# Kernel tuning notes

Hardware: AMD Instinct MI355X
Metric: run time of the kernel (lower is better)

Reference implementation:

```python
import jax, jax.numpy as jnp
import numpy as np

B = 8192       # number of windows (batch*windows_per_image)
N = 49         # tokens per 7x7 window
C = 128        # channels
H = 4          # heads
HD = C // H    # head dim = 32
WIN = (7, 7)


def _relative_position_index(win):
    wh, ww = win
    coords = np.stack(np.meshgrid(np.arange(wh), np.arange(ww), indexing='ij'))
    cf = coords.reshape(2, -1)                       # (2, N)
    rel = (cf[:, :, None] - cf[:, None, :]).transpose(1, 2, 0)  # (N, N, 2)
    rel[:, :, 0] += wh - 1
    rel[:, :, 1] += ww - 1
    rel[:, :, 0] *= 2 * ww - 1
    return jnp.array(rel.sum(-1).reshape(-1), dtype=jnp.int32)  # (N*N,)


def setup_inputs() -> dict:
    key = jax.random.key(0)
    ks = jax.random.split(key, 7)
    x = jax.random.normal(ks[0], (B, N, C), dtype=jnp.float32)
    mask = jax.random.normal(ks[1], (B, 1, N, N), dtype=jnp.float32)
    qkv_w = jax.random.normal(ks[2], (C, 3 * C), dtype=jnp.float32) * (C ** -0.5)
    qkv_b = jnp.zeros((3 * C,), dtype=jnp.float32)
    rel_bias_table = jax.random.normal(ks[3], ((2 * WIN[0] - 1) * (2 * WIN[1] - 1), H), dtype=jnp.float32)
    proj_w = jax.random.normal(ks[4], (C, C), dtype=jnp.float32) * (C ** -0.5)
    proj_b = jnp.zeros((C,), dtype=jnp.float32)
    rel_index = _relative_position_index(WIN)
    return {"x": x, "mask": mask, "qkv_w": qkv_w, "qkv_b": qkv_b,
            "rel_bias_table": rel_bias_table, "proj_w": proj_w,
            "proj_b": proj_b, "rel_index": rel_index}


def reference(x, mask, qkv_w, qkv_b, rel_bias_table, proj_w, proj_b, rel_index):
    b, n, c = x.shape
    scale = HD ** -0.5
    qkv = (x @ qkv_w + qkv_b).reshape(b, n, 3, H, HD).transpose(2, 0, 3, 1, 4)
    q, k, v = qkv[0] * scale, qkv[1], qkv[2]          # (b, H, n, HD)
    attn = jnp.einsum('bhqd,bhkd->bhqk', q, k)        # (b, H, n, n)
    # gathered relative position bias: (n*n, H) -> (1, H, n, n)
    bias = rel_bias_table[rel_index].reshape(n, n, H).transpose(2, 0, 1)[None]
    attn = jax.nn.softmax(attn + bias + mask, axis=-1)
    out = jnp.einsum('bhqk,bhkd->bhqd', attn, v)       # (b, H, n, HD)
    out = out.transpose(0, 2, 1, 3).reshape(b, n, c)
    return out @ proj_w + proj_b
```

## Files before the change

### kernel.cpp

```cpp
#include <hip/hip_runtime.h>
#include <hip/hip_bf16.h>

using f32x4 = __attribute__((ext_vector_type(4))) float;
using bf16x8 = __attribute__((ext_vector_type(8))) short;

#define DEVI __device__ __forceinline__

DEVI short f2bf(float f) { __hip_bfloat16 h = __float2bfloat16(f); return *reinterpret_cast<short*>(&h); }
DEVI unsigned int pk2(float a, float b) {
    float2 t; t.x = a; t.y = b;
    __hip_bfloat162 h = __float22bfloat162_rn(t);
    return *reinterpret_cast<unsigned int*>(&h);
}
DEVI float bf2f(unsigned short s) { unsigned int u = ((unsigned int)s) << 16; return __uint_as_float(u); }

DEVI void pl32swap(unsigned& a, unsigned& b) { asm("v_permlane32_swap_b32 %0, %1" : "+v"(a), "+v"(b)); }
DEVI void pl16swap(unsigned& a, unsigned& b) { asm("v_permlane16_swap_b32 %0, %1" : "+v"(a), "+v"(b)); }

#define GLOAD_LDS16(gp, lp) \
    __builtin_amdgcn_global_load_lds((const __attribute__((address_space(1))) void*)(gp), \
                                     (__attribute__((address_space(3))) void*)(lp), 16, 0, 0)

constexpr int NB = 8192;
constexpr int NT = 49;
constexpr int CD = 128;
constexpr float SCALE = 0.17677669529663687f;
constexpr float LOG2E = 1.4426950408889634f;

constexpr size_t WS_QKVWS  = 0;
constexpr size_t WS_PROJWT = 98304;
constexpr size_t WS_BIAS   = 131072;

DEVI void div49(unsigned grow, unsigned& bI, unsigned& tI) {
    bI = (unsigned)(((unsigned long long)grow * 2804876602ull) >> 37);
    tI = grow - bI * 49u;
}

DEVI int swz128(int row, int col) { return row * 128 + (col ^ ((row & 7) << 3)); }

__global__ __launch_bounds__(256) void prep_kernel(
    const float* __restrict__ qkv_w, const float* __restrict__ proj_w,
    const float* __restrict__ rbt, const int* __restrict__ rel_index,
    short* __restrict__ qkvwS, short* __restrict__ projwT, unsigned short* __restrict__ biasBf)
{
    int i = blockIdx.x * 256 + threadIdx.x;
    if (i < 384 * 128) {
        int n = i >> 7, j = i & 127;
        int c = n >> 7, r = n & 127;
        qkvwS[c * 16384 + r * 128 + (j ^ ((r & 7) << 3))] = f2bf(qkv_w[j * 384 + n]);
    }
    if (i < 128 * 128) {
        int n = i >> 7, j = i & 127;
        projwT[n * 128 + j] = f2bf(proj_w[j * 128 + n]);
    }
    if (i < 4 * NT * NT) {
        int h = i / (NT * NT); int t = i % (NT * NT);
        int k = t / NT, q = t - k * NT;
        biasBf[i] = (unsigned short)f2bf(rbt[rel_index[q * NT + k] * 4 + h] * LOG2E);
    }
}

__global__ __launch_bounds__(512, 4) void fused_kernel(
    const float* __restrict__ x, const float* __restrict__ mask,
    const float* __restrict__ qkv_b, const short* __restrict__ qkvwS,
    const unsigned short* __restrict__ biasT, const short* __restrict__ projwT,
    const float* __restrict__ proj_b, float* __restrict__ out)
{
    __shared__ __attribute__((aligned(16))) short pool[40960];
    char*  Wcb = (char*)pool;
    char*  qkb = (char*)pool + 32768;
    char*  vSb = (char*)pool + 65536;
    float* mT  = (float*)pool;
    short* oS  = (short*)((char*)pool + 49152);

    const int b = blockIdx.x;
    const int tid = threadIdx.x;
    const int w = tid >> 6, lane = tid & 63, lr = lane & 15, lg = lane >> 4;
    const int h = w >> 1, half = w & 1;
    const int wpair = w >> 1;
    const int tsel = w & 1;

    const float* mb_ = mask + (size_t)b * (NT * NT);
    float mreg[5];
#pragma unroll
    for (int ii = 0; ii < 5; ++ii) {
        int i = tid + ii * 512;
        mreg[ii] = (i < NT * NT) ? mb_[i] * LOG2E : 0.f;
    }

    bf16x8 af[2][4];
#pragma unroll
    for (int mf = 0; mf < 2; ++mf) {
        const int row = 32 * tsel + 16 * mf + lr;
        const bool valid = row < NT;
        const float* xrow = x + ((size_t)b * NT + (valid ? row : 0)) * CD;
#pragma unroll
        for (int kt = 0; kt < 4; ++kt) {
            float4 v0 = {0.f,0.f,0.f,0.f}, v1 = {0.f,0.f,0.f,0.f};
            if (valid) {
                const float4* p = reinterpret_cast<const float4*>(xrow + kt * 32 + lg * 8);
                v0 = p[0]; v1 = p[1];
            }
            union { unsigned int u[4]; bf16x8 v; } cv;
            cv.u[0] = pk2(v0.x, v0.y); cv.u[1] = pk2(v0.z, v0.w);
            cv.u[2] = pk2(v1.x, v1.y); cv.u[3] = pk2(v1.z, v1.w);
            af[mf][kt] = cv.v;
        }
    }

    const char* srcW = (const char*)qkvwS;
#pragma unroll
    for (int c = 0; c < 3; ++c) {
#pragma unroll
        for (int i = 0; i < 4; ++i)
            GLOAD_LDS16(srcW + c * 32768 + w * 4096 + i * 1024 + lane * 16,
                        Wcb + w * 4096 + i * 1024);
        __syncthreads();

        if (c < 2) {
#pragma unroll
            for (int nn = 0; nn < 2; ++nn) {
                const int ntl = wpair + 4 * nn;
                const int nt = c * 8 + ntl;
                const int hh = (ntl >> 1) & 3;
                const int dtile = ntl & 1;
                const float4 b4 = *reinterpret_cast<const float4*>(qkv_b + nt * 16 + 4 * lg);
                const float scl = (c == 0) ? SCALE * LOG2E : 1.0f;
                const char* wbase = Wcb + (ntl * 16 + lr) * 256;
                const int wsw = (lr & 7) << 4;
#pragma unroll
                for (int tf = 0; tf < 2; ++tf) {
                    f32x4 acc = {0.f, 0.f, 0.f, 0.f};
#pragma unroll
                    for (int kt = 0; kt < 4; ++kt) {
                        bf16x8 wf = *reinterpret_cast<const bf16x8*>(wbase + ((kt * 64 + lg * 16) ^ wsw));
                        acc = __builtin_amdgcn_mfma_f32_16x16x32_bf16(wf, af[tf][kt], acc, 0, 0, 0);
                    }
                    const int t = 16 * (2 * tsel + tf) + lr;
                    const int gp = (dtile * 4 + lg) ^ (t & 6);
                    uint2 s;
                    s.x = pk2((acc[0] + b4.x) * scl, (acc[1] + b4.y) * scl);
                    s.y = pk2((acc[2] + b4.z) * scl, (acc[3] + b4.w) * scl);
                    *reinterpret_cast<uint2*>(qkb + c * 16384 + hh * 4096 + t * 64 + gp * 8) = s;
                }
            }
        } else {
#pragma unroll
            for (int nn = 0; nn < 2; ++nn) {
                const int ntl = wpair + 4 * nn;
                const int nt = 16 + ntl;
                const int hh = (ntl >> 1) & 3;
                const int d0 = (ntl & 1) * 16;
                const float bv = qkv_b[nt * 16 + lr];
                const int d = d0 + lr;
                const char* wbase = Wcb + (ntl * 16 + lr) * 256;
                const int wsw = (lr & 7) << 4;
#pragma unroll
                for (int tf = 0; tf < 2; ++tf) {
                    f32x4 acc = {0.f, 0.f, 0.f, 0.f};
#pragma unroll
                    for (int kt = 0; kt < 4; ++kt) {
                        bf16x8 wf = *reinterpret_cast<const bf16x8*>(wbase + ((kt * 64 + lg * 16) ^ wsw));
                        acc = __builtin_amdgcn_mfma_f32_16x16x32_bf16(af[tf][kt], wf, acc, 0, 0, 0);
                    }
                    const int tt = 2 * tsel + tf;
                    const int slotq = (lg < 2) ? (tt * 8 + 4 * lg) : (24 + tt * 8 + 4 * lg);
                    const int gp = (slotq >> 2) ^ ((d & 7) << 1);
                    uint2 s;
                    s.x = pk2(acc[0] + bv, acc[1] + bv);
                    s.y = pk2(acc[2] + bv, acc[3] + bv);
                    *reinterpret_cast<uint2*>(vSb + hh * 4096 + d * 128 + gp * 8) = s;
                }
            }
        }
        __syncthreads();
    }

    const int mt0 = 2 * half;
    bf16x8 qa[2], kb[4];
#pragma unroll
    for (int i = 0; i < 2; ++i) {
        const int t = 16 * (mt0 + i) + lr;
        qa[i] = *reinterpret_cast<const bf16x8*>(qkb + h * 4096 + t * 64 + ((16 * lg) ^ ((t & 6) << 3)));
    }
#pragma unroll
    for (int t4 = 0; t4 < 4; ++t4) {
        const int t = 16 * t4 + lr;
        kb[t4] = *reinterpret_cast<const bf16x8*>(qkb + 16384 + h * 4096 + t * 64 + ((16 * lg) ^ ((t & 6) << 3)));
    }
#pragma unroll
    for (int ii = 0; ii < 5; ++ii) {
        int i = tid + ii * 512;
        if (i < NT * NT) {
            unsigned q_, k_;
            div49((unsigned)i, q_, k_);
            mT[k_ * 65 + q_] = mreg[ii];
        }
    }
    __syncthreads();

    const unsigned short* biasTh = biasT + h * (NT * NT);
    const short* vSs = (short*)vSb + h * 2048;
    const int sw8 = (lr & 7) << 3;

    f32x4 oacc[2][2];
#pragma unroll
    for (int mt2 = 0; mt2 < 2; ++mt2) { oacc[mt2][0] = f32x4{0,0,0,0}; oacc[mt2][1] = f32x4{0,0,0,0}; }

#pragma unroll
    for (int mt2 = 0; mt2 < 2; ++mt2) {
        const int qcol = 16 * (mt0 + mt2) + lr;

        float mbb[4][4];
#pragma unroll
        for (int ct = 0; ct < 4; ++ct)
#pragma unroll
            for (int r = 0; r < 4; ++r) {
                int k = 16 * ct + 4 * lg + r;
                int kc = min(k, 49);
                mbb[ct][r] = mT[kc * 65 + qcol] + bf2f(biasTh[kc * NT + qcol]);
            }

        f32x4 sacc[4];
#pragma unroll
        for (int ct = 0; ct < 4; ++ct) {
            f32x4 z = {0.f, 0.f, 0.f, 0.f};
            sacc[ct] = __builtin_amdgcn_mfma_f32_16x16x32_bf16(kb[ct], qa[mt2], z, 0, 0, 0);
        }

        float e[4][4];
        float psum = 0.f;
#pragma unroll
        for (int ct = 0; ct < 4; ++ct)
#pragma unroll
            for (int r = 0; r < 4; ++r) {
                float ee = exp2f(sacc[ct][r] + mbb[ct][r]);
                if (ct == 3) ee = (r == 0 && lg == 0) ? ee : 0.f;
                e[ct][r] = ee;
                psum += ee;
            }
        psum += __shfl_xor(psum, 16);
        psum += __shfl_xor(psum, 32);
        const float inv = 1.0f / psum;

        unsigned A0 = pk2(e[0][0] * inv, e[0][1] * inv);
        unsigned A1 = pk2(e[1][0] * inv, e[1][1] * inv);
        unsigned A2 = pk2(e[2][0] * inv, e[2][1] * inv);
        unsigned A3 = pk2(e[3][0] * inv, e[3][1] * inv);
        unsigned B0 = pk2(e[0][2] * inv, e[0][3] * inv);
        unsigned B1 = pk2(e[1][2] * inv, e[1][3] * inv);
        unsigned B2 = pk2(e[2][2] * inv, e[2][3] * inv);
        unsigned B3 = pk2(e[3][2] * inv, e[3][3] * inv);
        pl32swap(A0, A2); pl32swap(A1, A3);
        pl16swap(A0, A1); pl16swap(A2, A3);
        pl32swap(B0, B2); pl32swap(B1, B3);
        pl16swap(B0, B1); pl16swap(B2, B3);
        union { unsigned u[4]; bf16x8 v; } p0, p1;
        p0.u[0] = A0; p0.u[1] = B0; p0.u[2] = A1; p0.u[3] = B1;
        p1.u[0] = A2; p1.u[1] = B2; p1.u[2] = A3; p1.u[3] = B3;

#pragma unroll
        for (int nt = 0; nt < 2; ++nt) {
            bf16x8 vb0 = *reinterpret_cast<const bf16x8*>(&vSs[(16 * nt + lr) * 64 + ((8 * lg) ^ sw8)]);
            bf16x8 vb1 = *reinterpret_cast<const bf16x8*>(&vSs[(16 * nt + lr) * 64 + ((32 + 8 * lg) ^ sw8)]);
            oacc[mt2][nt] = __builtin_amdgcn_mfma_f32_16x16x32_bf16(p0.v, vb0, oacc[mt2][nt], 0, 0, 0);
            oacc[mt2][nt] = __builtin_amdgcn_mfma_f32_16x16x32_bf16(p1.v, vb1, oacc[mt2][nt], 0, 0, 0);
        }
    }

#pragma unroll
    for (int mt2 = 0; mt2 < 2; ++mt2)
#pragma unroll
        for (int nt = 0; nt < 2; ++nt)
#pragma unroll
            for (int r = 0; r < 4; ++r) {
                int row = 16 * (mt0 + mt2) + 4 * lg + r;
                int col = 32 * h + 16 * nt + lr;
                oS[swz128(row, col)] = f2bf(oacc[mt2][nt][r]);
            }
    __syncthreads();

    {
        bf16x8 bbf[4];
        const short* brow = projwT + (w * 16 + lr) * 128 + lg * 8;
#pragma unroll
        for (int kt = 0; kt < 4; ++kt)
            bbf[kt] = *reinterpret_cast<const bf16x8*>(brow + kt * 32);

        f32x4 acc[4];
#pragma unroll
        for (int mf = 0; mf < 4; ++mf) acc[mf] = f32x4{0.f, 0.f, 0.f, 0.f};

#pragma unroll
        for (int mf = 0; mf < 4; ++mf)
#pragma unroll
            for (int kt = 0; kt < 4; ++kt) {
                bf16x8 a2 = *reinterpret_cast<const bf16x8*>(&oS[swz128(16 * mf + lr, kt * 32 + lg * 8)]);
                acc[mf] = __builtin_amdgcn_mfma_f32_16x16x32_bf16(a2, bbf[kt], acc[mf], 0, 0, 0);
            }

        const int col = w * 16 + lr;
        const float pb = proj_b[col];
#pragma unroll
        for (int mf = 0; mf < 4; ++mf)
#pragma unroll
            for (int r = 0; r < 4; ++r) {
                int row = 16 * mf + 4 * lg + r;
                if (row < NT)
                    out[((size_t)b * NT + row) * CD + col] = acc[mf][r] + pb;
            }
    }
}

extern "C" void kernel_launch(void* const* d_in, const int* in_sizes, int n_in,
                              void* d_out, int out_size, void* d_ws, size_t ws_size,
                              hipStream_t stream) {
    const float* x      = (const float*)d_in[0];
    const float* mask   = (const float*)d_in[1];
    const float* qkv_w  = (const float*)d_in[2];
    const float* qkv_b  = (const float*)d_in[3];
    const float* rbt    = (const float*)d_in[4];
    const float* proj_w = (const float*)d_in[5];
    const float* proj_b = (const float*)d_in[6];
    const int*   ridx   = (const int*)d_in[7];
    float* out = (float*)d_out;

    char* ws = (char*)d_ws;
    short* qkvwS  = (short*)(ws + WS_QKVWS);
    short* projwT = (short*)(ws + WS_PROJWT);
    unsigned short* biasBf = (unsigned short*)(ws + WS_BIAS);

    prep_kernel<<<192, 256, 0, stream>>>(qkv_w, proj_w, rbt, ridx, qkvwS, projwT, biasBf);
    fused_kernel<<<NB, 512, 0, stream>>>(x, mask, qkv_b, qkvwS, biasBf, projwT, proj_b, out);
}
```

Baseline: 292.6 us.

## Load mask and bias directly into registers, drop LDS mask transpose

```diff
diff --git a/kernel.cpp b/kernel.cpp
--- a/kernel.cpp
+++ b/kernel.cpp
@@ -30,11 +30,6 @@
 constexpr size_t WS_QKVWS  = 0;
 constexpr size_t WS_PROJWT = 98304;
 constexpr size_t WS_BIAS   = 131072;
-
-DEVI void div49(unsigned grow, unsigned& bI, unsigned& tI) {
-    bI = (unsigned)(((unsigned long long)grow * 2804876602ull) >> 37);
-    tI = grow - bI * 49u;
-}
 
 DEVI int swz128(int row, int col) { return row * 128 + (col ^ ((row & 7) << 3)); }
 
@@ -70,7 +65,6 @@
     char*  Wcb = (char*)pool;
     char*  qkb = (char*)pool + 32768;
     char*  vSb = (char*)pool + 65536;
-    float* mT  = (float*)pool;
     short* oS  = (short*)((char*)pool + 49152);
 
     const int b = blockIdx.x;
@@ -79,14 +73,6 @@
     const int h = w >> 1, half = w & 1;
     const int wpair = w >> 1;
     const int tsel = w & 1;
-
-    const float* mb_ = mask + (size_t)b * (NT * NT);
-    float mreg[5];
-#pragma unroll
-    for (int ii = 0; ii < 5; ++ii) {
-        int i = tid + ii * 512;
-        mreg[ii] = (i < NT * NT) ? mb_[i] * LOG2E : 0.f;
-    }
 
     bf16x8 af[2][4];
 #pragma unroll
@@ -137,7 +123,7 @@
                         acc = __builtin_amdgcn_mfma_f32_16x16x32_bf16(wf, af[tf][kt], acc, 0, 0, 0);
                     }
                     const int t = 16 * (2 * tsel + tf) + lr;
-                    const int gp = (dtile * 4 + lg) ^ (t & 6);
+                    const int gp = (dtile * 4 + lg) ^ (t & 6) ^ ((t & 8) >> 1);
                     uint2 s;
                     s.x = pk2((acc[0] + b4.x) * scl, (acc[1] + b4.y) * scl);
                     s.y = pk2((acc[2] + b4.z) * scl, (acc[3] + b4.w) * scl);
@@ -177,29 +163,39 @@
     }
 
     const int mt0 = 2 * half;
+    const float* mb_ = mask + (size_t)b * (NT * NT);
+    const unsigned short* biasTh = biasT + h * (NT * NT);
     bf16x8 qa[2], kb[4];
 #pragma unroll
     for (int i = 0; i < 2; ++i) {
         const int t = 16 * (mt0 + i) + lr;
-        qa[i] = *reinterpret_cast<const bf16x8*>(qkb + h * 4096 + t * 64 + ((16 * lg) ^ ((t & 6) << 3)));
+        qa[i] = *reinterpret_cast<const bf16x8*>(
+            qkb + h * 4096 + t * 64 + ((16 * lg) ^ ((t & 6) << 3) ^ ((t & 8) << 2)));
     }
 #pragma unroll
     for (int t4 = 0; t4 < 4; ++t4) {
         const int t = 16 * t4 + lr;
-        kb[t4] = *reinterpret_cast<const bf16x8*>(qkb + 16384 + h * 4096 + t * 64 + ((16 * lg) ^ ((t & 6) << 3)));
-    }
-#pragma unroll
-    for (int ii = 0; ii < 5; ++ii) {
-        int i = tid + ii * 512;
-        if (i < NT * NT) {
-            unsigned q_, k_;
-            div49((unsigned)i, q_, k_);
-            mT[k_ * 65 + q_] = mreg[ii];
-        }
+        kb[t4] = *reinterpret_cast<const bf16x8*>(
+            qkb + 16384 + h * 4096 + t * 64 + ((16 * lg) ^ ((t & 6) << 3) ^ ((t & 8) << 2)));
+    }
+    float mraw[2][4][4];
+    unsigned short braw[2][4][4];
+#pragma unroll
+    for (int mt2 = 0; mt2 < 2; ++mt2) {
+        const int qc = min(16 * (mt0 + mt2) + lr, 48);
+        const float* mrow = mb_ + (size_t)qc * NT;
+        const unsigned short* brow = biasTh + qc;
+#pragma unroll
+        for (int ct = 0; ct < 4; ++ct)
+#pragma unroll
+            for (int r = 0; r < 4; ++r) {
+                int kc = min(16 * ct + 4 * lg + r, 48);
+                mraw[mt2][ct][r] = mrow[kc];
+                braw[mt2][ct][r] = brow[kc * NT];
+            }
     }
     __syncthreads();
 
-    const unsigned short* biasTh = biasT + h * (NT * NT);
     const short* vSs = (short*)vSb + h * 2048;
     const int sw8 = (lr & 7) << 3;
 
@@ -209,18 +205,6 @@
 
 #pragma unroll
     for (int mt2 = 0; mt2 < 2; ++mt2) {
-        const int qcol = 16 * (mt0 + mt2) + lr;
-
-        float mbb[4][4];
-#pragma unroll
-        for (int ct = 0; ct < 4; ++ct)
-#pragma unroll
-            for (int r = 0; r < 4; ++r) {
-                int k = 16 * ct + 4 * lg + r;
-                int kc = min(k, 49);
-                mbb[ct][r] = mT[kc * 65 + qcol] + bf2f(biasTh[kc * NT + qcol]);
-            }
-
         f32x4 sacc[4];
 #pragma unroll
         for (int ct = 0; ct < 4; ++ct) {
@@ -234,7 +218,8 @@
         for (int ct = 0; ct < 4; ++ct)
 #pragma unroll
             for (int r = 0; r < 4; ++r) {
-                float ee = exp2f(sacc[ct][r] + mbb[ct][r]);
+                float sv = sacc[ct][r] + fmaf(mraw[mt2][ct][r], LOG2E, bf2f(braw[mt2][ct][r]));
+                float ee = exp2f(sv);
                 if (ct == 3) ee = (r == 0 && lg == 0) ? ee : 0.f;
                 e[ct][r] = ee;
                 psum += ee;
@@ -268,6 +253,14 @@
         }
     }
 
+    bf16x8 bbf[4];
+    {
+        const short* brow = projwT + (w * 16 + lr) * 128 + lg * 8;
+#pragma unroll
+        for (int kt = 0; kt < 4; ++kt)
+            bbf[kt] = *reinterpret_cast<const bf16x8*>(brow + kt * 32);
+    }
+
 #pragma unroll
     for (int mt2 = 0; mt2 < 2; ++mt2)
 #pragma unroll
@@ -281,12 +274,6 @@
     __syncthreads();
 
     {
-        bf16x8 bbf[4];
-        const short* brow = projwT + (w * 16 + lr) * 128 + lg * 8;
-#pragma unroll
-        for (int kt = 0; kt < 4; ++kt)
-            bbf[kt] = *reinterpret_cast<const bf16x8*>(brow + kt * 32);
-
         f32x4 acc[4];
 #pragma unroll
         for (int mf = 0; mf < 4; ++mf) acc[mf] = f32x4{0.f, 0.f, 0.f, 0.f};
```

After: 297.7 us. No clear change (+1.7%).
